# Performance work log

Hardware: AMD Instinct MI355X
Metric: run time of the kernel (lower is better)

## Reference

```python
import jax, jax.numpy as jnp
import numpy as np


def _scatter_mean(vals, idx, num_segments):
    # torch_scatter.scatter_mean semantics: sum per segment / count, count clamped to >=1
    s = jax.ops.segment_sum(vals, idx, num_segments=num_segments)
    cnt = jax.ops.segment_sum(jnp.ones((vals.shape[0],), vals.dtype), idx, num_segments=num_segments)
    return s / jnp.maximum(cnt, 1.0)[:, None]


def setup_inputs() -> dict:
    key = jax.random.key(0)
    k1, k2, k3, k4 = jax.random.split(key, 4)
    E, IN, OUT, N = 1600000, 64, 64, 100000
    edge_emb = jax.random.normal(k1, (E, IN), dtype=jnp.float32)
    edge_index = jax.random.randint(k2, (2, E), 0, N, dtype=jnp.int32)
    # Linear params (Kaiming-uniform-ish scale is irrelevant for correctness baseline)
    W = jax.random.normal(k3, (IN, OUT), dtype=jnp.float32) / np.sqrt(IN)
    b = jax.random.normal(k4, (OUT,), dtype=jnp.float32) * 0.01
    return {"edge_emb": edge_emb, "edge_index": edge_index, "num_nodes": N, "W": W, "b": b}


def reference(edge_emb, edge_index, num_nodes, W, b):
    src, dst = edge_index[0], edge_index[1]
    h = jax.nn.relu(edge_emb @ W + b)           # [E, out] (proj computed once; same math as calling it twice)
    msg_src = _scatter_mean(h, src, num_nodes)  # [N, out]
    msg_dst = _scatter_mean(h, dst, num_nodes)  # [N, out]
    return 0.5 * (msg_src + msg_dst)
```

## Files before the change

### kernel.cpp

```cpp
#include <hip/hip_runtime.h>


__global__ __launch_bounds__(256, 4) void edge_scatter_kernel(
    const float* __restrict__ x,
    const int*   __restrict__ src,
    const int*   __restrict__ dst,
    const float* __restrict__ W,
    const float* __restrict__ bias,
    float* __restrict__ sum_src,
    float* __restrict__ sum_dst,
    float* __restrict__ cnt_src,
    float* __restrict__ cnt_dst,
    int E)
{
    const int lane          = threadIdx.x & 63;
    const int wave_in_blk   = threadIdx.x >> 6;
    const int waves_per_blk = blockDim.x >> 6;
    const int gwave  = blockIdx.x * waves_per_blk + wave_in_blk;
    const int nwaves = gridDim.x * waves_per_blk;

    float w[64];
#pragma unroll
    for (int k = 0; k < 64; ++k) w[k] = W[k * 64 + lane];
    const float bj = bias[lane];

    for (int e = gwave; e < E; e += nwaves) {
        const int eu = __builtin_amdgcn_readfirstlane(e);
        const int s = src[eu];
        const int d = dst[eu];
        const float4* __restrict__ xr4 =
            (const float4*)(x + (size_t)eu * 64);

        float a0 = bj, a1 = 0.0f, a2 = 0.0f, a3 = 0.0f;
#pragma unroll
        for (int k4 = 0; k4 < 16; ++k4) {
            const float4 v = xr4[k4];
            a0 = fmaf(v.x, w[4 * k4 + 0], a0);
            a1 = fmaf(v.y, w[4 * k4 + 1], a1);
            a2 = fmaf(v.z, w[4 * k4 + 2], a2);
            a3 = fmaf(v.w, w[4 * k4 + 3], a3);
        }
        const float h = fmaxf((a0 + a1) + (a2 + a3), 0.0f);

        atomicAdd(sum_src + (size_t)s * 64 + lane, h);
        atomicAdd(sum_dst + (size_t)d * 64 + lane, h);
        if (lane == 0) {
            atomicAdd(cnt_src + s, 1.0f);
            atomicAdd(cnt_dst + d, 1.0f);
        }
    }
}

__global__ __launch_bounds__(256) void combine_kernel(
    const float4* __restrict__ sum_src4,
    const float4* __restrict__ sum_dst4,
    const float*  __restrict__ cnt_src,
    const float*  __restrict__ cnt_dst,
    float4* __restrict__ out4,
    int total4)
{
    int i = blockIdx.x * blockDim.x + threadIdx.x;
    if (i >= total4) return;
    int n = i >> 4;
    float rs = 0.5f / fmaxf(cnt_src[n], 1.0f);
    float rd = 0.5f / fmaxf(cnt_dst[n], 1.0f);
    float4 a = sum_src4[i];
    float4 b = sum_dst4[i];
    float4 o;
    o.x = a.x * rs + b.x * rd;
    o.y = a.y * rs + b.y * rd;
    o.z = a.z * rs + b.z * rd;
    o.w = a.w * rs + b.w * rd;
    out4[i] = o;
}

extern "C" void kernel_launch(void* const* d_in, const int* in_sizes, int n_in,
                              void* d_out, int out_size, void* d_ws, size_t ws_size,
                              hipStream_t stream)
{
    const float* x  = (const float*)d_in[0];
    const int*   ei = (const int*)d_in[1];
    const float* W  = (const float*)d_in[3];
    const float* b  = (const float*)d_in[4];

    const int E = in_sizes[0] / 64;
    const int N = out_size / 64;

    float* sum_src = (float*)d_ws;
    float* sum_dst = sum_src + (size_t)N * 64;
    float* cnt_src = sum_dst + (size_t)N * 64;
    float* cnt_dst = cnt_src + N;

    size_t zero_bytes = ((size_t)N * 128 + 2 * (size_t)N) * sizeof(float);
    hipMemsetAsync(d_ws, 0, zero_bytes, stream);

    const int* srcp = ei;
    const int* dstp = ei + E;

    edge_scatter_kernel<<<1280, 256, 0, stream>>>(
        x, srcp, dstp, W, b, sum_src, sum_dst, cnt_src, cnt_dst, E);

    const int total4 = (N * 64) / 4;
    combine_kernel<<<(total4 + 255) / 256, 256, 0, stream>>>(
        (const float4*)sum_src, (const float4*)sum_dst, cnt_src, cnt_dst,
        (float4*)d_out, total4);
}
```

Before: 1.391 ms.

## Replace atomic scatter with CSR build and per-node gather that recomputes projections

Builds CSR adjacency for src and dst nodes via histogram, prefix scan and fill kernels. A per-node gather kernel then recomputes each incident edge's projected features and averages them, writing the output directly without float atomics. This removes the large volume of float atomic traffic and the combine pass. In exchange, the projection is computed twice per edge, edge rows are read in random order, and several extra preprocessing kernels run each call.

```diff
diff --git a/kernel.cpp b/kernel.cpp
--- a/kernel.cpp
+++ b/kernel.cpp
@@ -1,17 +1,125 @@
 #include <hip/hip_runtime.h>
 
 
-__global__ __launch_bounds__(256, 4) void edge_scatter_kernel(
+__global__ __launch_bounds__(256) void hist_kernel(
+    const int* __restrict__ ei, int* __restrict__ cnt, int twoE, int E, int N)
+{
+    int i = blockIdx.x * blockDim.x + threadIdx.x;
+    int stride = gridDim.x * blockDim.x;
+    for (; i < twoE; i += stride) {
+        int node = ei[i] + ((i < E) ? 0 : N);
+        atomicAdd(&cnt[node], 1);
+    }
+}
+
+__global__ __launch_bounds__(1024) void scan_partial_kernel(
+    const int* __restrict__ cnt, int* __restrict__ offl,
+    int* __restrict__ bsum, int n)
+{
+    __shared__ int s[1024];
+    const int t = threadIdx.x;
+    const int i = blockIdx.x * 1024 + t;
+    const int v = (i < n) ? cnt[i] : 0;
+    s[t] = v;
+    __syncthreads();
+#pragma unroll
+    for (int st = 1; st < 1024; st <<= 1) {
+        int add = (t >= st) ? s[t - st] : 0;
+        __syncthreads();
+        s[t] += add;
+        __syncthreads();
+    }
+    if (i < n) offl[i] = s[t] - v;
+    if (t == 1023) bsum[blockIdx.x] = s[t];
+}
+
+__global__ __launch_bounds__(1024) void scan_blocks_kernel(int* bsum, int B)
+{
+    __shared__ int s[1024];
+    const int t = threadIdx.x;
+    const int v = (t < B) ? bsum[t] : 0;
+    s[t] = v;
+    __syncthreads();
+#pragma unroll
+    for (int st = 1; st < 1024; st <<= 1) {
+        int add = (t >= st) ? s[t - st] : 0;
+        __syncthreads();
+        s[t] += add;
+        __syncthreads();
+    }
+    if (t < B) bsum[t] = s[t] - v;
+}
+
+__global__ __launch_bounds__(256) void finalize_kernel(
+    const int* __restrict__ offl, const int* __restrict__ bsum,
+    int* __restrict__ off, int* __restrict__ cur, int n)
+{
+    int i = blockIdx.x * blockDim.x + threadIdx.x;
+    if (i >= n) return;
+    int o = offl[i] + bsum[i >> 10];
+    off[i] = o;
+    cur[i] = o;
+}
+
+__global__ __launch_bounds__(256) void fill_kernel(
+    const int* __restrict__ ei, int* __restrict__ cur,
+    int* __restrict__ adj, int twoE, int E, int N)
+{
+    int i = blockIdx.x * blockDim.x + threadIdx.x;
+    int stride = gridDim.x * blockDim.x;
+    for (; i < twoE; i += stride) {
+        int node = ei[i] + ((i < E) ? 0 : N);
+        int pos = atomicAdd(&cur[node], 1);
+        adj[pos] = (i < E) ? i : (i - E);
+    }
+}
+
+__device__ __forceinline__ float edge_h(const float* __restrict__ xrow,
+                                        const float w[64], float bj)
+{
+    const float4* __restrict__ r = (const float4*)xrow;
+    float a0 = bj, a1 = 0.f, a2 = 0.f, a3 = 0.f;
+#pragma unroll
+    for (int k4 = 0; k4 < 16; ++k4) {
+        const float4 v = r[k4];
+        a0 = fmaf(v.x, w[4 * k4 + 0], a0);
+        a1 = fmaf(v.y, w[4 * k4 + 1], a1);
+        a2 = fmaf(v.z, w[4 * k4 + 2], a2);
+        a3 = fmaf(v.w, w[4 * k4 + 3], a3);
+    }
+    return fmaxf((a0 + a1) + (a2 + a3), 0.f);
+}
+
+__device__ __forceinline__ float seg_accum(const float* __restrict__ x,
+                                           const int* __restrict__ adj,
+                                           int base, int c,
+                                           const float w[64], float bj)
+{
+    float acc = 0.f;
+    int i = 0;
+    for (; i + 2 <= c; i += 2) {
+        int e0 = __builtin_amdgcn_readfirstlane(adj[base + i]);
+        int e1 = __builtin_amdgcn_readfirstlane(adj[base + i + 1]);
+        float h0 = edge_h(x + (size_t)e0 * 64, w, bj);
+        float h1 = edge_h(x + (size_t)e1 * 64, w, bj);
+        acc += h0 + h1;
+    }
+    if (i < c) {
+        int e0 = __builtin_amdgcn_readfirstlane(adj[base + i]);
+        acc += edge_h(x + (size_t)e0 * 64, w, bj);
+    }
+    return acc;
+}
+
+__global__ __launch_bounds__(256) void gather_kernel(
     const float* __restrict__ x,
-    const int*   __restrict__ src,
-    const int*   __restrict__ dst,
+    const int*   __restrict__ adj,
+    const int*   __restrict__ off,
+    const int*   __restrict__ cnt,
     const float* __restrict__ W,
     const float* __restrict__ bias,
-    float* __restrict__ sum_src,
-    float* __restrict__ sum_dst,
-    float* __restrict__ cnt_src,
-    float* __restrict__ cnt_dst,
-    int E)
+    float* __restrict__ out,
+    int N)
 {
     const int lane          = threadIdx.x & 63;
     const int wave_in_blk   = threadIdx.x >> 6;
@@ -24,54 +132,15 @@
     for (int k = 0; k < 64; ++k) w[k] = W[k * 64 + lane];
     const float bj = bias[lane];
 
-    for (int e = gwave; e < E; e += nwaves) {
-        const int eu = __builtin_amdgcn_readfirstlane(e);
-        const int s = src[eu];
-        const int d = dst[eu];
-        const float4* __restrict__ xr4 =
-            (const float4*)(x + (size_t)eu * 64);
-
-        float a0 = bj, a1 = 0.0f, a2 = 0.0f, a3 = 0.0f;
-#pragma unroll
-        for (int k4 = 0; k4 < 16; ++k4) {
-            const float4 v = xr4[k4];
-            a0 = fmaf(v.x, w[4 * k4 + 0], a0);
-            a1 = fmaf(v.y, w[4 * k4 + 1], a1);
-            a2 = fmaf(v.z, w[4 * k4 + 2], a2);
-            a3 = fmaf(v.w, w[4 * k4 + 3], a3);
-        }
-        const float h = fmaxf((a0 + a1) + (a2 + a3), 0.0f);
-
-        atomicAdd(sum_src + (size_t)s * 64 + lane, h);
-        atomicAdd(sum_dst + (size_t)d * 64 + lane, h);
-        if (lane == 0) {
-            atomicAdd(cnt_src + s, 1.0f);
-            atomicAdd(cnt_dst + d, 1.0f);
-        }
+    for (int n = gwave; n < N; n += nwaves) {
+        const int b0 = off[n],     c0 = cnt[n];
+        const int b1 = off[N + n], c1 = cnt[N + n];
+        const float a_s = seg_accum(x, adj, b0, c0, w, bj);
+        const float a_d = seg_accum(x, adj, b1, c1, w, bj);
+        const float r = 0.5f * (a_s / fmaxf((float)c0, 1.f) +
+                                a_d / fmaxf((float)c1, 1.f));
+        out[(size_t)n * 64 + lane] = r;
     }
-}
-
-__global__ __launch_bounds__(256) void combine_kernel(
-    const float4* __restrict__ sum_src4,
-    const float4* __restrict__ sum_dst4,
-    const float*  __restrict__ cnt_src,
-    const float*  __restrict__ cnt_dst,
-    float4* __restrict__ out4,
-    int total4)
-{
-    int i = blockIdx.x * blockDim.x + threadIdx.x;
-    if (i >= total4) return;
-    int n = i >> 4;
-    float rs = 0.5f / fmaxf(cnt_src[n], 1.0f);
-    float rd = 0.5f / fmaxf(cnt_dst[n], 1.0f);
-    float4 a = sum_src4[i];
-    float4 b = sum_dst4[i];
-    float4 o;
-    o.x = a.x * rs + b.x * rd;
-    o.y = a.y * rs + b.y * rd;
-    o.z = a.z * rs + b.z * rd;
-    o.w = a.w * rs + b.w * rd;
-    out4[i] = o;
 }
 
 extern "C" void kernel_launch(void* const* d_in, const int* in_sizes, int n_in,
@@ -83,25 +152,29 @@
     const float* W  = (const float*)d_in[3];
     const float* b  = (const float*)d_in[4];
 
-    const int E = in_sizes[0] / 64;
-    const int N = out_size / 64;
+    const int E    = in_sizes[0] / 64;
+    const int N    = out_size / 64;
+    const int twoE = 2 * E;
+    const int twoN = 2 * N;
 
-    float* sum_src = (float*)d_ws;
-    float* sum_dst = sum_src + (size_t)N * 64;
-    float* cnt_src = sum_dst + (size_t)N * 64;
-    float* cnt_dst = cnt_src + N;
+    int* cnt  = (int*)d_ws;
+    int* offl = cnt  + twoN;
+    int* off  = offl + twoN;
+    int* cur  = off  + twoN;
+    int* bsum = cur  + twoN;
+    int* adj  = bsum + 1024;
 
-    size_t zero_bytes = ((size_t)N * 128 + 2 * (size_t)N) * sizeof(float);
-    hipMemsetAsync(d_ws, 0, zero_bytes, stream);
+    hipMemsetAsync(cnt, 0, (size_t)twoN * sizeof(int), stream);
 
-    const int* srcp = ei;
-    const int* dstp = ei + E;
+    hist_kernel<<<2048, 256, 0, stream>>>(ei, cnt, twoE, E, N);
 
-    edge_scatter_kernel<<<1280, 256, 0, stream>>>(
-        x, srcp, dstp, W, b, sum_src, sum_dst, cnt_src, cnt_dst, E);
+    const int B = (twoN + 1023) / 1024;
+    scan_partial_kernel<<<B, 1024, 0, stream>>>(cnt, offl, bsum, twoN);
+    scan_blocks_kernel<<<1, 1024, 0, stream>>>(bsum, B);
+    finalize_kernel<<<(twoN + 255) / 256, 256, 0, stream>>>(offl, bsum, off, cur, twoN);
 
-    const int total4 = (N * 64) / 4;
-    combine_kernel<<<(total4 + 255) / 256, 256, 0, stream>>>(
-        (const float4*)sum_src, (const float4*)sum_dst, cnt_src, cnt_dst,
-        (float4*)d_out, total4);
+    fill_kernel<<<2048, 256, 0, stream>>>(ei, cur, adj, twoE, E, N);
+
+    gather_kernel<<<2560, 256, 0, stream>>>(x, adj, off, cnt, W, b,
+                                            (float*)d_out, N);
 }
```

Result: slower. 1.767 ms (+27.1%).
